# Performance work log

Measured on AMD Instinct MI355X. Metric: run time of the kernel, lower is better.

## Reference

```python
import jax, jax.numpy as jnp
import numpy as np
from jax import lax

B, N, C = 8, 4096, 64
RATIO = 0.25
M = int(N * RATIO)          # sampled centers per cloud (fps ratio)
K = 64                      # max_num_neighbors in ball query
R = 0.2                     # ball_query_radius
H = 128                     # MLP width
NEG = jnp.float32(-1e30)


def setup_inputs() -> dict:
    key = jax.random.key(0)
    k1, k2, k3, k4 = jax.random.split(key, 4)
    x = jax.random.normal(k1, (B, N, C), jnp.float32)
    pos = jax.random.uniform(k2, (B, N, 3), jnp.float32)  # unit cube coords
    W1 = jax.random.normal(k3, (C + 3, H), jnp.float32) * 0.05
    b1 = jnp.zeros((H,), jnp.float32)
    W2 = jax.random.normal(k4, (H, H), jnp.float32) * 0.05
    b2 = jnp.zeros((H,), jnp.float32)
    return {"x": x, "pos": pos, "W1": W1, "b1": b1, "W2": W2, "b2": b2}


def _fps(pos):
    """Farthest point sampling on one cloud [N,3] -> M int32 indices (start at 0)."""
    d0 = jnp.sum((pos - pos[0]) ** 2, axis=-1)  # min sq-dist to selected set
    def step(mind, _):
        nxt = jnp.argmax(mind).astype(jnp.int32)
        d = jnp.sum((pos - pos[nxt]) ** 2, axis=-1)
        return jnp.minimum(mind, d), nxt
    _, idxs = lax.scan(step, d0, None, length=M - 1)
    return jnp.concatenate([jnp.zeros((1,), jnp.int32), idxs])


def reference(x, pos, W1, b1, W2, b2):
    # --- FPS sampling (per cloud, deterministic start) ---
    idx = jax.vmap(_fps)(pos)                      # [B,M]
    bidx = jnp.arange(B)[:, None]
    centers = pos[bidx, idx]                        # [B,M,3]

    # --- ball query: first K points within radius R of each center ---
    d2 = jnp.sum((centers[:, :, None, :] - pos[:, None, :, :]) ** 2, axis=-1)  # [B,M,N]
    in_ball = d2 <= R * R
    # prefer lowest index (torch_cluster radius returns up to K arbitrary/first hits)
    score = jnp.where(in_ball, -jnp.arange(N, dtype=jnp.float32), NEG)
    vals, nbr = lax.top_k(score, K)                 # nbr: [B,M,K] neighbor indices
    valid = vals > NEG / 2                          # [B,M,K]; center itself always valid

    # --- PointNetConv: gather -> local MLP on [x_j, pos_j - pos_i] -> max aggr ---
    b3 = jnp.arange(B)[:, None, None]
    xj = x[b3, nbr]                                  # [B,M,K,C]
    rel = pos[b3, nbr] - centers[:, :, None, :]      # [B,M,K,3]
    feat = jnp.concatenate([xj, rel], axis=-1)       # [B,M,K,C+3]
    h = jax.nn.relu(feat @ W1 + b1)
    h = jax.nn.relu(h @ W2 + b2)                     # [B,M,K,H]
    h = jnp.where(valid[..., None], h, NEG)
    out = jnp.max(h, axis=2)                          # [B,M,H] max aggregation
    return out, centers
```

## Files before the change

kernel.cpp:

```cpp
#include <hip/hip_runtime.h>

#define BN 8
#define NN 4096
#define CC 64
#define MM 1024
#define KK 64
#define HH 128

typedef __attribute__((ext_vector_type(8))) short short8;
typedef __attribute__((ext_vector_type(4))) float f32x4;
typedef __attribute__((ext_vector_type(2))) float f32x2;
typedef __attribute__((ext_vector_type(2))) double f64x2;
typedef unsigned long long u64;
typedef unsigned int u32;

__device__ inline unsigned short f2bf(float f) {
  union { float f; unsigned u; } v; v.f = f;
  unsigned r = v.u + 0x7FFFu + ((v.u >> 16) & 1u);
  return (unsigned short)(r >> 16);
}

__device__ inline float sqd(float ax, float ay, float az, float bx, float by, float bz) {
  float dx = __fsub_rn(ax, bx), dy = __fsub_rn(ay, by), dz = __fsub_rn(az, bz);
  return __fadd_rn(__fadd_rn(__fmul_rn(dx, dx), __fmul_rn(dy, dy)), __fmul_rn(dz, dz));
}

__global__ void prep_w(const float* __restrict__ W1, const float* __restrict__ W2,
                       short* __restrict__ W1T, short* __restrict__ W2T) {
  int t = blockIdx.x * 256 + threadIdx.x;
  if (t < 128 * 104) {
    int n = t / 104, k = t % 104;
    float v = (k < 67) ? W1[k * 128 + n] : 0.f;
    W1T[t] = (short)f2bf(v);
  }
  if (t < 128 * 136) {
    int n = t / 136, k = t % 136;
    float v = (k < 128) ? W2[k * 128 + n] : 0.f;
    W2T[t] = (short)f2bf(v);
  }
}

template <int CTRL, int RM>
__device__ __forceinline__ float dppf(float x) {
  int v = __builtin_amdgcn_update_dpp(0, __float_as_int(x), CTRL, RM, 0xF, false);
  return __int_as_float(v);
}

__device__ __forceinline__ float wave_fmax(float x) {
  x = fmaxf(x, dppf<0xB1, 0xF>(x));
  x = fmaxf(x, dppf<0x4E, 0xF>(x));
  x = fmaxf(x, dppf<0x141, 0xF>(x));
  x = fmaxf(x, dppf<0x140, 0xF>(x));
  x = fmaxf(x, dppf<0x142, 0xA>(x));
  x = fmaxf(x, dppf<0x143, 0xC>(x));
  return __int_as_float(__builtin_amdgcn_readlane(__float_as_int(x), 63));
}

__global__ __launch_bounds__(512) void fps_k(const float* __restrict__ pos,
                                             float* __restrict__ centers) {
  const int b = blockIdx.x;
  const int tid = threadIdx.x;
  const int lane = tid & 63;
  const int wv = tid >> 6;
  __shared__ __align__(16) double svk[2][8];
  __shared__ __align__(16) f32x4 sp4[NN];
  __shared__ float scen[MM * 3];

  const float* P = pos + (size_t)b * NN * 3;

  f32x2 X[4], Y[4], Z[4], M[4];
  {
    const f32x4* Pv = (const f32x4*)(P + (size_t)tid * 24);
    f32x4 v0 = Pv[0], v1 = Pv[1], v2 = Pv[2], v3 = Pv[3], v4 = Pv[4], v5 = Pv[5];
    X[0].x = v0[0]; Y[0].x = v0[1]; Z[0].x = v0[2];
    X[0].y = v0[3]; Y[0].y = v1[0]; Z[0].y = v1[1];
    X[1].x = v1[2]; Y[1].x = v1[3]; Z[1].x = v2[0];
    X[1].y = v2[1]; Y[1].y = v2[2]; Z[1].y = v2[3];
    X[2].x = v3[0]; Y[2].x = v3[1]; Z[2].x = v3[2];
    X[2].y = v3[3]; Y[2].y = v4[0]; Z[2].y = v4[1];
    X[3].x = v4[2]; Y[3].x = v4[3]; Z[3].x = v5[0];
    X[3].y = v5[1]; Y[3].y = v5[2]; Z[3].y = v5[3];
  }
#pragma unroll
  for (int j = 0; j < 4; ++j) {
    int p0 = tid * 8 + 2 * j;
    f32x4 w;
    w[0] = X[j].x; w[1] = Y[j].x; w[2] = Z[j].x; w[3] = 0.f; sp4[p0] = w;
    w[0] = X[j].y; w[1] = Y[j].y; w[2] = Z[j].y; w[3] = 0.f; sp4[p0 + 1] = w;
  }
#pragma unroll
  for (int j = 0; j < 4; ++j)
    asm volatile("" : "+v"(X[j]), "+v"(Y[j]), "+v"(Z[j]));

  const float c0x = P[0], c0y = P[1], c0z = P[2];
  if (tid == 0) { scen[0] = c0x; scen[1] = c0y; scen[2] = c0z; }
  f32x2 E;
  float mv;
  {
#pragma clang fp contract(off)
    f32x2 vcx; vcx.x = c0x; vcx.y = c0x;
    f32x2 vcy; vcy.x = c0y; vcy.y = c0y;
    f32x2 vcz; vcz.x = c0z; vcz.y = c0z;
#pragma unroll
    for (int j = 0; j < 4; ++j) {
      f32x2 dx = X[j] - vcx, dy = Y[j] - vcy, dz = Z[j] - vcz;
      M[j] = (dx * dx + dy * dy) + dz * dz;
    }
    f32x2 A0 = __builtin_elementwise_max(M[0], M[1]);
    f32x2 A1 = __builtin_elementwise_max(M[2], M[3]);
    E = __builtin_elementwise_max(A0, A1);
    mv = fmaxf(E.x, E.y);
  }
  __syncthreads();

  for (int m = 1; m < MM; ++m) {
    const int pp = m & 1;
    float wmax = wave_fmax(mv);
    u64 bal = __ballot(mv == wmax);
    int L = (int)__builtin_ctzll(bal);
    u32 e = 7u;
    if (M[3].y == mv) e = 7u;
    if (M[3].x == mv) e = 6u;
    if (M[2].y == mv) e = 5u;
    if (M[2].x == mv) e = 4u;
    if (M[1].y == mv) e = 3u;
    if (M[1].x == mv) e = 2u;
    if (M[0].y == mv) e = 1u;
    if (M[0].x == mv) e = 0u;
    if (lane == L) {
      u64 key = ((u64)__float_as_uint(mv) << 32) | (u64)(u32)~(u32)(tid * 8 + e);
      svk[pp][wv] = __builtin_bit_cast(double, key);
    }
    __syncthreads();
    const f64x2* kd = (const f64x2*)&svk[pp][0];
    f64x2 k0 = kd[0], k1 = kd[1], k2 = kd[2], k3 = kd[3];
    double q0 = fmax(k0.x, k0.y), q1 = fmax(k1.x, k1.y);
    double q2 = fmax(k2.x, k2.y), q3 = fmax(k3.x, k3.y);
    double kb = fmax(fmax(q0, q1), fmax(q2, q3));
    u32 bp = ~(u32)__builtin_bit_cast(u64, kb);
    f32x4 c4 = sp4[bp];
    if (tid == 0) {
      scen[m * 3 + 0] = c4[0];
      scen[m * 3 + 1] = c4[1];
      scen[m * 3 + 2] = c4[2];
    }
    {
#pragma clang fp contract(off)
      f32x2 vcx; vcx.x = c4[0]; vcx.y = c4[0];
      f32x2 vcy; vcy.x = c4[1]; vcy.y = c4[1];
      f32x2 vcz; vcz.x = c4[2]; vcz.y = c4[2];
#pragma unroll
      for (int j = 0; j < 4; ++j) {
        f32x2 dx = X[j] - vcx, dy = Y[j] - vcy, dz = Z[j] - vcz;
        f32x2 d2 = (dx * dx + dy * dy) + dz * dz;
        M[j] = __builtin_elementwise_min(M[j], d2);
      }
      f32x2 A0 = __builtin_elementwise_max(M[0], M[1]);
      f32x2 A1 = __builtin_elementwise_max(M[2], M[3]);
      E = __builtin_elementwise_max(A0, A1);
      mv = fmaxf(E.x, E.y);
    }
  }
  __syncthreads();
  for (int i = tid; i < MM * 3; i += 512)
    centers[(size_t)b * MM * 3 + i] = scen[i];
}

__global__ __launch_bounds__(256) void sa_k(const float* __restrict__ x,
                                            const float* __restrict__ pos,
                                            const float* __restrict__ b1,
                                            const float* __restrict__ b2,
                                            const short* __restrict__ W1T,
                                            const short* __restrict__ W2T,
                                            const float* __restrict__ centers,
                                            float* __restrict__ out) {
  const int cm = blockIdx.x;
  const int b = cm >> 10;
  const int tid = threadIdx.x;
  const int lane = tid & 63, wv = tid >> 6;
  const int l15 = lane & 15, lg = lane >> 4;

  __shared__ short s_feat[64][104];
  __shared__ short s_h1[64][136];
  __shared__ int s_nbr[64];
  __shared__ int s_wcnt[4];

  const int n0 = wv * 32;
  short8 w1f[2][3], w2f[2][4];
#pragma unroll
  for (int nt = 0; nt < 2; ++nt) {
    int row = n0 + nt * 16 + l15;
#pragma unroll
    for (int kt = 0; kt < 3; ++kt)
      w1f[nt][kt] = *reinterpret_cast<const short8*>(W1T + row * 104 + kt * 32 + lg * 8);
#pragma unroll
    for (int kt = 0; kt < 4; ++kt)
      w2f[nt][kt] = *reinterpret_cast<const short8*>(W2T + row * 136 + kt * 32 + lg * 8);
  }

  const float* Pb = pos + (size_t)b * NN * 3;
  const float cx = centers[(size_t)cm * 3 + 0];
  const float cy = centers[(size_t)cm * 3 + 1];
  const float cz = centers[(size_t)cm * 3 + 2];

  int cnt = 0;
  for (int base = 0; base < NN; base += 256) {
    int p = base + tid;
    float d2 = sqd(Pb[p * 3 + 0], Pb[p * 3 + 1], Pb[p * 3 + 2], cx, cy, cz);
    bool pred = d2 <= 0.04f;
    unsigned long long mask = __ballot(pred);
    if (lane == 0) s_wcnt[wv] = __popcll(mask);
    __syncthreads();
    int wbase = cnt, tot = 0;
#pragma unroll
    for (int w = 0; w < 4; ++w) {
      int c = s_wcnt[w];
      tot += c;
      if (w < wv) wbase += c;
    }
    if (pred) {
      int slot = wbase + (int)__popcll(mask & ((1ull << lane) - 1ull));
      if (slot < KK) s_nbr[slot] = p;
    }
    cnt += tot;
    __syncthreads();
    if (cnt >= KK) break;
  }
  if (cnt > KK) cnt = KK;

  {
    int* fz = (int*)&s_feat[0][0];
    for (int i = tid; i < 64 * 104 / 2; i += 256) fz[i] = 0;
  }
  __syncthreads();

  {
    const int j = tid >> 2, q = tid & 3;
    if (j < cnt) {
      int nj = s_nbr[j];
      const float* xr = x + ((size_t)b * NN + nj) * CC + q * 16;
      unsigned* dst = (unsigned*)&s_feat[j][q * 16];
#pragma unroll
      for (int v4 = 0; v4 < 4; ++v4) {
        f32x4 xv = *reinterpret_cast<const f32x4*>(xr + v4 * 4);
        unsigned lo0 = (unsigned)f2bf(xv[0]) | ((unsigned)f2bf(xv[1]) << 16);
        unsigned lo1 = (unsigned)f2bf(xv[2]) | ((unsigned)f2bf(xv[3]) << 16);
        dst[v4 * 2 + 0] = lo0;
        dst[v4 * 2 + 1] = lo1;
      }
      if (q == 0) {
        s_feat[j][64] = (short)f2bf(__fsub_rn(Pb[nj * 3 + 0], cx));
        s_feat[j][65] = (short)f2bf(__fsub_rn(Pb[nj * 3 + 1], cy));
        s_feat[j][66] = (short)f2bf(__fsub_rn(Pb[nj * 3 + 2], cz));
      }
    }
  }
  __syncthreads();

  f32x4 acc[4][2];
#pragma unroll
  for (int mt = 0; mt < 4; ++mt)
#pragma unroll
    for (int nt = 0; nt < 2; ++nt) acc[mt][nt] = (f32x4)0.f;

#pragma unroll
  for (int mt = 0; mt < 4; ++mt) {
    int arow = mt * 16 + l15;
#pragma unroll
    for (int kt = 0; kt < 3; ++kt) {
      short8 af = *reinterpret_cast<const short8*>(&s_feat[arow][kt * 32 + lg * 8]);
      acc[mt][0] = __builtin_amdgcn_mfma_f32_16x16x32_bf16(af, w1f[0][kt], acc[mt][0], 0, 0, 0);
      acc[mt][1] = __builtin_amdgcn_mfma_f32_16x16x32_bf16(af, w1f[1][kt], acc[mt][1], 0, 0, 0);
    }
  }

#pragma unroll
  for (int mt = 0; mt < 4; ++mt) {
#pragma unroll
    for (int nt = 0; nt < 2; ++nt) {
      int col = n0 + nt * 16 + l15;
      float bias = b1[col];
#pragma unroll
      for (int r = 0; r < 4; ++r) {
        int row = mt * 16 + lg * 4 + r;
        float h = fmaxf(__fadd_rn(acc[mt][nt][r], bias), 0.f);
        s_h1[row][col] = (short)f2bf(h);
      }
    }
  }
  __syncthreads();

  f32x4 acc2[4][2];
#pragma unroll
  for (int mt = 0; mt < 4; ++mt)
#pragma unroll
    for (int nt = 0; nt < 2; ++nt) acc2[mt][nt] = (f32x4)0.f;

#pragma unroll
  for (int mt = 0; mt < 4; ++mt) {
    int arow = mt * 16 + l15;
#pragma unroll
    for (int kt = 0; kt < 4; ++kt) {
      short8 af = *reinterpret_cast<const short8*>(&s_h1[arow][kt * 32 + lg * 8]);
      acc2[mt][0] = __builtin_amdgcn_mfma_f32_16x16x32_bf16(af, w2f[0][kt], acc2[mt][0], 0, 0, 0);
      acc2[mt][1] = __builtin_amdgcn_mfma_f32_16x16x32_bf16(af, w2f[1][kt], acc2[mt][1], 0, 0, 0);
    }
  }

#pragma unroll
  for (int nt = 0; nt < 2; ++nt) {
    int col = n0 + nt * 16 + l15;
    float bias = b2[col];
    float mx = -1e30f;
#pragma unroll
    for (int mt = 0; mt < 4; ++mt) {
#pragma unroll
      for (int r = 0; r < 4; ++r) {
        int row = mt * 16 + lg * 4 + r;
        float h = fmaxf(__fadd_rn(acc2[mt][nt][r], bias), 0.f);
        if (row < cnt) mx = fmaxf(mx, h);
      }
    }
    mx = fmaxf(mx, __shfl_xor(mx, 16));
    mx = fmaxf(mx, __shfl_xor(mx, 32));
    if (lg == 0) out[(size_t)cm * HH + col] = mx;
  }
}

extern "C" void kernel_launch(void* const* d_in, const int* in_sizes, int n_in,
                              void* d_out, int out_size, void* d_ws, size_t ws_size,
                              hipStream_t stream) {
  const float* x = (const float*)d_in[0];
  const float* pos = (const float*)d_in[1];
  const float* W1 = (const float*)d_in[2];
  const float* b1 = (const float*)d_in[3];
  const float* W2 = (const float*)d_in[4];
  const float* b2 = (const float*)d_in[5];

  float* out = (float*)d_out;
  float* centers = out + (size_t)BN * MM * HH;

  char* ws = (char*)d_ws;
  short* W1T = (short*)ws;
  short* W2T = (short*)(ws + 26624);

  prep_w<<<68, 256, 0, stream>>>(W1, W2, W1T, W2T);
  fps_k<<<BN, 512, 0, stream>>>(pos, centers);
  sa_k<<<BN * MM, 256, 0, stream>>>(x, pos, b1, b2, W1T, W2T, centers, out);
}
```

Before: 693.6 us.

## Scan all points in one pass for ball query and remap block order

```diff
diff --git a/kernel.cpp b/kernel.cpp
--- a/kernel.cpp
+++ b/kernel.cpp
@@ -54,6 +54,53 @@
   x = fmaxf(x, dppf<0x142, 0xA>(x));
   x = fmaxf(x, dppf<0x143, 0xC>(x));
   return __int_as_float(__builtin_amdgcn_readlane(__float_as_int(x), 63));
+}
+
+__device__ __forceinline__ int wave_iscan_add(int c) {
+  int v = c;
+  v += __builtin_amdgcn_update_dpp(0, v, 0x111, 0xF, 0xF, true);
+  v += __builtin_amdgcn_update_dpp(0, v, 0x112, 0xF, 0xF, true);
+  v += __builtin_amdgcn_update_dpp(0, v, 0x114, 0xF, 0xF, true);
+  v += __builtin_amdgcn_update_dpp(0, v, 0x118, 0xF, 0xF, true);
+  v += __builtin_amdgcn_update_dpp(0, v, 0x142, 0xA, 0xF, true);
+  v += __builtin_amdgcn_update_dpp(0, v, 0x143, 0xC, 0xF, true);
+  return v;
+}
+
+__device__ __forceinline__ void load8(const float* Pl, f32x2 (&X)[4], f32x2 (&Y)[4],
+                                      f32x2 (&Z)[4]) {
+  f32x4 v0 = *(const f32x4*)(Pl + 0);
+  f32x4 v1 = *(const f32x4*)(Pl + 4);
+  f32x4 v2 = *(const f32x4*)(Pl + 8);
+  f32x4 v3 = *(const f32x4*)(Pl + 12);
+  f32x4 v4 = *(const f32x4*)(Pl + 16);
+  f32x4 v5 = *(const f32x4*)(Pl + 20);
+  X[0].x = v0[0]; Y[0].x = v0[1]; Z[0].x = v0[2];
+  X[0].y = v0[3]; Y[0].y = v1[0]; Z[0].y = v1[1];
+  X[1].x = v1[2]; Y[1].x = v1[3]; Z[1].x = v2[0];
+  X[1].y = v2[1]; Y[1].y = v2[2]; Z[1].y = v2[3];
+  X[2].x = v3[0]; Y[2].x = v3[1]; Z[2].x = v3[2];
+  X[2].y = v3[3]; Y[2].y = v4[0]; Z[2].y = v4[1];
+  X[3].x = v4[2]; Y[3].x = v4[3]; Z[3].x = v5[0];
+  X[3].y = v5[1]; Y[3].y = v5[2]; Z[3].y = v5[3];
+}
+
+__device__ __forceinline__ u32 hit8(const float* Pl, float cx, float cy, float cz) {
+#pragma clang fp contract(off)
+  f32x2 X[4], Y[4], Z[4];
+  load8(Pl, X, Y, Z);
+  f32x2 vcx; vcx.x = cx; vcx.y = cx;
+  f32x2 vcy; vcy.x = cy; vcy.y = cy;
+  f32x2 vcz; vcz.x = cz; vcz.y = cz;
+  u32 h = 0;
+#pragma unroll
+  for (int j = 0; j < 4; ++j) {
+    f32x2 dx = X[j] - vcx, dy = Y[j] - vcy, dz = Z[j] - vcz;
+    f32x2 d2 = (dx * dx + dy * dy) + dz * dz;
+    if (d2.x <= 0.04f) h |= 1u << (2 * j);
+    if (d2.y <= 0.04f) h |= 1u << (2 * j + 1);
+  }
+  return h;
 }
 
 __global__ __launch_bounds__(512) void fps_k(const float* __restrict__ pos,
@@ -119,16 +166,16 @@
     u64 bal = __ballot(mv == wmax);
     int L = (int)__builtin_ctzll(bal);
     u32 e = 7u;
-    if (M[3].y == mv) e = 7u;
-    if (M[3].x == mv) e = 6u;
-    if (M[2].y == mv) e = 5u;
-    if (M[2].x == mv) e = 4u;
-    if (M[1].y == mv) e = 3u;
-    if (M[1].x == mv) e = 2u;
-    if (M[0].y == mv) e = 1u;
-    if (M[0].x == mv) e = 0u;
+    if (M[3].y == wmax) e = 7u;
+    if (M[3].x == wmax) e = 6u;
+    if (M[2].y == wmax) e = 5u;
+    if (M[2].x == wmax) e = 4u;
+    if (M[1].y == wmax) e = 3u;
+    if (M[1].x == wmax) e = 2u;
+    if (M[0].y == wmax) e = 1u;
+    if (M[0].x == wmax) e = 0u;
     if (lane == L) {
-      u64 key = ((u64)__float_as_uint(mv) << 32) | (u64)(u32)~(u32)(tid * 8 + e);
+      u64 key = ((u64)__float_as_uint(wmax) << 32) | (u64)(u32)~(u32)(tid * 8 + (int)e);
       svk[pp][wv] = __builtin_bit_cast(double, key);
     }
     __syncthreads();
@@ -174,7 +221,8 @@
                                             const short* __restrict__ W2T,
                                             const float* __restrict__ centers,
                                             float* __restrict__ out) {
-  const int cm = blockIdx.x;
+  const int bid = blockIdx.x;
+  const int cm = (bid & 7) * 1024 + (bid >> 3);
   const int b = cm >> 10;
   const int tid = threadIdx.x;
   const int lane = tid & 63, wv = tid >> 6;
@@ -203,34 +251,32 @@
   const float cy = centers[(size_t)cm * 3 + 1];
   const float cz = centers[(size_t)cm * 3 + 2];
 
-  int cnt = 0;
-  for (int base = 0; base < NN; base += 256) {
-    int p = base + tid;
-    float d2 = sqd(Pb[p * 3 + 0], Pb[p * 3 + 1], Pb[p * 3 + 2], cx, cy, cz);
-    bool pred = d2 <= 0.04f;
-    unsigned long long mask = __ballot(pred);
-    if (lane == 0) s_wcnt[wv] = __popcll(mask);
-    __syncthreads();
-    int wbase = cnt, tot = 0;
-#pragma unroll
-    for (int w = 0; w < 4; ++w) {
-      int c = s_wcnt[w];
-      tot += c;
-      if (w < wv) wbase += c;
-    }
-    if (pred) {
-      int slot = wbase + (int)__popcll(mask & ((1ull << lane) - 1ull));
-      if (slot < KK) s_nbr[slot] = p;
-    }
-    cnt += tot;
-    __syncthreads();
-    if (cnt >= KK) break;
-  }
-  if (cnt > KK) cnt = KK;
-
+  const int q0 = tid * 16;
+  u32 hm = hit8(Pb + (size_t)q0 * 3, cx, cy, cz)
+         | (hit8(Pb + (size_t)q0 * 3 + 24, cx, cy, cz) << 8);
+  int c = __popc(hm);
+  int inc = wave_iscan_add(c);
+  if (lane == 63) s_wcnt[wv] = inc;
+  __syncthreads();
+  int woff = 0, tot = 0;
+#pragma unroll
+  for (int w = 0; w < 4; ++w) {
+    int t = s_wcnt[w];
+    tot += t;
+    if (w < wv) woff += t;
+  }
+  int cnt = tot > KK ? KK : tot;
+  int slot = woff + inc - c;
   {
     int* fz = (int*)&s_feat[0][0];
     for (int i = tid; i < 64 * 104 / 2; i += 256) fz[i] = 0;
+  }
+#pragma unroll
+  for (int i = 0; i < 16; ++i) {
+    if (hm & (1u << i)) {
+      if (slot < KK) s_nbr[slot] = q0 + i;
+      ++slot;
+    }
   }
   __syncthreads();
 
```

Measured after the change: 676.3 us (median of 2 runs). 2.5% less time.
